# Kernel optimization log

Hardware: AMD Instinct MI355X
Metric: run time of the kernel (lower is better)

The kernel has to match this reference:

```python
import math
import jax, jax.numpy as jnp
import numpy as np

NUM_HEADS = 16
HEAD_DIM = 128
BLOCK = 256
EPS = 1e-6


def _get_slopes(n):
    def p2(n):
        start = 2 ** (-2 ** (-(math.log2(n) - 3)))
        return [start * start ** i for i in range(n)]
    if math.log2(n).is_integer():
        return p2(n)
    c = 2 ** math.floor(math.log2(n))
    return p2(c) + _get_slopes(2 * c)[0::2][: n - c]


def setup_inputs() -> dict:
    key = jax.random.key(0)
    ks = jax.random.split(key, 4)
    d_in, d_out = 2048, 2048
    x = jax.random.normal(ks[0], (2, 4096, d_in), dtype=jnp.float32)
    Wqkv = jax.random.normal(ks[1], (d_in, 3 * NUM_HEADS * HEAD_DIM), dtype=jnp.float32) * 0.02
    Wg = jax.random.normal(ks[2], (d_in, NUM_HEADS * HEAD_DIM), dtype=jnp.float32) * 0.02
    Wout = jax.random.normal(ks[3], (NUM_HEADS * HEAD_DIM, d_out), dtype=jnp.float32) * 0.02
    norm_w = jnp.ones((NUM_HEADS * HEAD_DIM,), dtype=jnp.float32)
    return {"x": x, "Wqkv": Wqkv, "Wg": Wg, "Wout": Wout, "norm_w": norm_w}


def reference(x, Wqkv, Wg, Wout, norm_w):
    b, n, _ = x.shape
    h, d = NUM_HEADS, HEAD_DIM
    nb = n // BLOCK  # seq_len chosen divisible by block_size

    # slopes (ALiBi-style), shape [h,1,1]
    slope = jnp.asarray(_get_slopes(h), dtype=jnp.float32).reshape(h, 1, 1)

    qkv = jax.nn.silu(x @ Wqkv)                       # [b,n,3hd]
    qkv = qkv.reshape(b, n, h, 3 * d)
    q, k, v = jnp.split(qkv, 3, axis=-1)              # each [b,n,h,d]
    q = q.transpose(0, 2, 1, 3)                       # [b,h,n,d]
    k = k.transpose(0, 2, 1, 3)
    v = v.transpose(0, 2, 1, 3)

    # per-position decay factors within a block
    arr = jnp.arange(BLOCK, dtype=jnp.float32) + 1.0          # [B]
    q_decay = jnp.exp(-slope * arr[:, None])                  # [h,B,1]
    k_decay = jnp.exp(-slope * (BLOCK - arr[:, None]))        # [h,B,1]
    idx = arr[:, None] - arr[None, :]                         # [B,B]
    diag_decay = jnp.where(idx >= 0, jnp.exp(-slope[None] * idx[None, None]), 0.0)  # [1,h,B,B]
    block_decay = jnp.exp(-slope * BLOCK)                     # [h,1,1]

    # blocked xs: [nb, b, h, B, d]
    def to_blocks(t):
        return t.reshape(b, h, nb, BLOCK, d).transpose(2, 0, 1, 3, 4)

    qb, kb, vb = to_blocks(q), to_blocks(k), to_blocks(v)

    def step(kv, blk):
        qi, ki, vi = blk                                       # [b,h,B,d]
        # inter-block: (qi * q_decay) @ kv  -> [b,h,B,d]
        non_diag = jnp.einsum('bhmd,bhde->bhme', qi * q_decay, kv)
        # intra-block causal decayed attention
        qk = jnp.einsum('bhmd,bhnd->bhmn', qi, ki) * diag_decay
        diag = jnp.einsum('bhmn,bhne->bhme', qk, vi)
        out = non_diag + diag
        kv_new = block_decay * kv + jnp.einsum('bhmd,bhme->bhde', ki * k_decay, vi)
        return kv_new, out

    kv0 = jnp.zeros((b, h, d, d), dtype=jnp.float32)
    _, out_blocks = jax.lax.scan(step, kv0, (qb, kb, vb))      # [nb,b,h,B,d]
    o = out_blocks.transpose(1, 2, 0, 3, 4).reshape(b, h, n, d)
    o = o.transpose(0, 2, 1, 3).reshape(b, n, h * d)           # [b,n,hd]

    # T5 (RMS) LayerNorm
    var = jnp.mean(o * o, axis=-1, keepdims=True)
    o = o * jax.lax.rsqrt(var + EPS) * norm_w

    # output gate and projection
    o = jax.nn.sigmoid(x @ Wg) * o
    return o @ Wout
```

## Files before the change

### kernel.cpp

```cpp
#include <hip/hip_runtime.h>
#include <cstddef>

typedef float f32x4 __attribute__((ext_vector_type(4)));
typedef __bf16 bf16x8 __attribute__((ext_vector_type(8)));
typedef unsigned short u16x8 __attribute__((ext_vector_type(8)));
typedef unsigned short u16x4 __attribute__((ext_vector_type(4)));

constexpr int NB = 2, S = 4096, H = 16, D = 128;
constexpr int DIN = 2048, NQKV = 6144, HD = 2048;
constexpr int BLK = 256, NBL = 16;

constexpr size_t SZ_XB    = (size_t)NB * S * DIN * 2;
constexpr size_t SZ_WQKVT = (size_t)NQKV * DIN * 2;
constexpr size_t SZ_WGT   = (size_t)HD * DIN * 2;
constexpr size_t SZ_WOUTT = (size_t)HD * HD * 2;
constexpr size_t SZ_QKVB  = (size_t)NB * S * NQKV * 2;
constexpr size_t SZ_GB    = (size_t)NB * S * HD * 2;
constexpr size_t SZ_ST    = (size_t)NB * H * NBL * D * D * 2;
constexpr size_t SZ_OB    = (size_t)NB * S * HD * 2;

__device__ __forceinline__ float bf2f(unsigned short u) {
  return __uint_as_float(((unsigned)u) << 16);
}
__device__ __forceinline__ unsigned short f2bf(float f) {
  unsigned u = __float_as_uint(f);
  u += 0x7fffu + ((u >> 16) & 1u);
  return (unsigned short)(u >> 16);
}
__device__ __forceinline__ void gload16(const void* g, void* l) {
  __builtin_amdgcn_global_load_lds(
      (const __attribute__((address_space(1))) unsigned int*)g,
      (__attribute__((address_space(3))) unsigned int*)l, 16, 0, 0);
}

__global__ __launch_bounds__(256) void cvt_bf16(
    const float* __restrict__ in, unsigned short* __restrict__ out) {
  const size_t id = (size_t)blockIdx.x * 256 + threadIdx.x;
  const float4 a = *(const float4*)&in[id * 8];
  const float4 c = *(const float4*)&in[id * 8 + 4];
  u16x8 o;
  o[0] = f2bf(a.x); o[1] = f2bf(a.y); o[2] = f2bf(a.z); o[3] = f2bf(a.w);
  o[4] = f2bf(c.x); o[5] = f2bf(c.y); o[6] = f2bf(c.z); o[7] = f2bf(c.w);
  *(u16x8*)&out[id * 8] = o;
}

__global__ __launch_bounds__(256) void transpose_cvt(
    const float* __restrict__ W, unsigned short* __restrict__ Wt, int K, int N) {
  __shared__ unsigned short tile[32][33];
  const int n0 = blockIdx.x * 32, k0 = blockIdx.y * 32;
  const int t = threadIdx.x;
  const int r = t >> 3, c4 = (t & 7) * 4;
  const float4 v = *(const float4*)&W[(size_t)(k0 + r) * N + n0 + c4];
  tile[r][c4 + 0] = f2bf(v.x);
  tile[r][c4 + 1] = f2bf(v.y);
  tile[r][c4 + 2] = f2bf(v.z);
  tile[r][c4 + 3] = f2bf(v.w);
  __syncthreads();
  u16x4 o;
  #pragma unroll
  for (int i = 0; i < 4; ++i) o[i] = tile[c4 + i][r];
  *(u16x4*)&Wt[(size_t)(n0 + r) * K + k0 + c4] = o;
}

template<int ACT>
__global__ __launch_bounds__(256, 4) void gemm128(
    const unsigned short* __restrict__ A, const unsigned short* __restrict__ Bt,
    void* __restrict__ O1, void* __restrict__ O2,
    int M, int N, int K, int NSPLIT) {
  __shared__ unsigned short lds[16384];
  char* ldsb = (char*)lds;
  const int t = threadIdx.x;
  const int lane = t & 63, wave = t >> 6;
  const int wr = wave >> 1, wc = wave & 1;
  const int l15 = lane & 15;

  const int nbm = M >> 7;
  const int nbmx = nbm >> 3;
  const int xcd = blockIdx.x & 7, q = blockIdx.x >> 3;
  const int bm = xcd * nbmx + (q % nbmx);
  const int bn = q / nbmx;

  const int cg = (t & 7) ^ ((t >> 3) & 7);
  const unsigned short* sA = A  + (size_t)(bm * 128 + (t >> 3)) * K + cg * 8;
  const unsigned short* sB = Bt + (size_t)(bn * 128 + (t >> 3)) * K + cg * 8;
  const int dstb = t << 4;

  int offA[2][4], offB[2][4];
  #pragma unroll
  for (int kk = 0; kk < 2; ++kk) {
    #pragma unroll
    for (int m = 0; m < 4; ++m) {
      const int row = wr * 64 + m * 16 + l15;
      offA[kk][m] = row * 128 + (((kk * 4 + (lane >> 4)) ^ (row & 7)) << 4);
    }
    #pragma unroll
    for (int n = 0; n < 4; ++n) {
      const int row = wc * 64 + n * 16 + l15;
      offB[kk][n] = 16384 + row * 128 + (((kk * 4 + (lane >> 4)) ^ (row & 7)) << 4);
    }
  }

  const int NT = K >> 6;
  f32x4 acc[4][4] = {};
  for (int u = 0; u < NT; ++u) {
    __syncthreads();
    const int ko = u * 64;
    #pragma unroll
    for (int i = 0; i < 4; ++i) {
      gload16(sA + (size_t)(i * 32) * K + ko, ldsb + i * 4096 + dstb);
      gload16(sB + (size_t)(i * 32) * K + ko, ldsb + 16384 + i * 4096 + dstb);
    }
    asm volatile("s_waitcnt vmcnt(0)" ::: "memory");
    __syncthreads();
    #pragma unroll
    for (int kk = 0; kk < 2; ++kk) {
      bf16x8 af[4], bfr[4];
      #pragma unroll
      for (int m = 0; m < 4; ++m) af[m] = *(const bf16x8*)(ldsb + offA[kk][m]);
      #pragma unroll
      for (int n = 0; n < 4; ++n) bfr[n] = *(const bf16x8*)(ldsb + offB[kk][n]);
      #pragma unroll
      for (int m = 0; m < 4; ++m)
        #pragma unroll
        for (int n = 0; n < 4; ++n)
          acc[m][n] = __builtin_amdgcn_mfma_f32_16x16x32_bf16(af[m], bfr[n], acc[m][n], 0, 0, 0);
    }
  }

  const int ro = (lane >> 4) * 4, co = l15;
  const bool lo = (bn * 128) < NSPLIT;
  #pragma unroll
  for (int m = 0; m < 4; ++m)
    #pragma unroll
    for (int n = 0; n < 4; ++n) {
      const int gc = bn * 128 + wc * 64 + n * 16 + co;
      #pragma unroll
      for (int r = 0; r < 4; ++r) {
        const int gr = bm * 128 + wr * 64 + m * 16 + ro + r;
        float v = acc[m][n][r];
        if constexpr (ACT == 0) {
          ((float*)O1)[(size_t)gr * N + gc] = v;
        } else {
          if (lo) {
            v = v / (1.f + __expf(-v));
            ((unsigned short*)O1)[(size_t)gr * NSPLIT + gc] = f2bf(v);
          } else {
            v = 1.f / (1.f + __expf(-v));
            ((unsigned short*)O2)[(size_t)gr * (N - NSPLIT) + (gc - NSPLIT)] = f2bf(v);
          }
        }
      }
    }
}

__global__ __launch_bounds__(256) void kv_outer(
    const unsigned short* __restrict__ qkv, unsigned short* __restrict__ st) {
  const int gid = blockIdx.x;
  const int j = gid & 15;
  const int bh = gid >> 4;
  const int h = bh & 15;
  const int b = bh >> 4;
  const float slope = exp2f(-0.5f * (float)(h + 1));
  const int t = threadIdx.x;
  const int lane = t & 63, wave = t >> 6, wr = wave >> 1, wc = wave & 1;
  const int l15 = lane & 15;
  __shared__ unsigned short vt[128][72];
  __shared__ unsigned short kt[128][72];
  f32x4 acc[4][4] = {};
  const int mm = t & 63;
  const int c0 = (t >> 6) * 32;
  for (int ch = 0; ch < 4; ++ch) {
    if (ch) __syncthreads();
    const int m = ch * 64 + mm;
    const int seq = b * S + j * BLK + m;
    const float kd = expf(-slope * (float)(255 - m));
    const unsigned short* row = &qkv[(size_t)seq * NQKV + h * 384];
    #pragma unroll
    for (int i = 0; i < 4; ++i) {
      const u16x8 k8 = *(const u16x8*)&row[128 + c0 + i * 8];
      const u16x8 v8 = *(const u16x8*)&row[256 + c0 + i * 8];
      #pragma unroll
      for (int q2 = 0; q2 < 8; ++q2) {
        kt[c0 + i * 8 + q2][mm] = f2bf(bf2f(k8[q2]) * kd);
        vt[c0 + i * 8 + q2][mm] = v8[q2];
      }
    }
    __syncthreads();
    #pragma unroll
    for (int kk = 0; kk < 2; ++kk) {
      bf16x8 af[4], bfr[4];
      #pragma unroll
      for (int mi = 0; mi < 4; ++mi)
        af[mi] = *(const bf16x8*)&vt[wr * 64 + mi * 16 + l15][kk * 32 + (lane >> 4) * 8];
      #pragma unroll
      for (int n = 0; n < 4; ++n)
        bfr[n] = *(const bf16x8*)&kt[wc * 64 + n * 16 + l15][kk * 32 + (lane >> 4) * 8];
      #pragma unroll
      for (int mi = 0; mi < 4; ++mi)
        #pragma unroll
        for (int n = 0; n < 4; ++n)
          acc[mi][n] = __builtin_amdgcn_mfma_f32_16x16x32_bf16(af[mi], bfr[n], acc[mi][n], 0, 0, 0);
    }
  }
  const size_t base = (size_t)gid * (D * D);
  const int ro = (lane >> 4) * 4;
  #pragma unroll
  for (int mi = 0; mi < 4; ++mi)
    #pragma unroll
    for (int n = 0; n < 4; ++n) {
      const int e = wc * 64 + n * 16 + l15;
      #pragma unroll
      for (int r = 0; r < 4; ++r) {
        const int f = wr * 64 + mi * 16 + ro + r;
        st[base + (size_t)f * D + e] = f2bf(acc[mi][n][r]);
      }
    }
}

__global__ __launch_bounds__(256) void kv_scan(unsigned short* __restrict__ st) {
  const int id = blockIdx.x * 256 + threadIdx.x;
  const int ef = id & (D * D - 1);
  const int bh = id >> 14;
  const int h = bh & 15;
  const float slope = exp2f(-0.5f * (float)(h + 1));
  const float bd = expf(-slope * 256.f);
  unsigned short* p = st + (size_t)bh * NBL * D * D + ef;
  float cur = 0.f;
  #pragma unroll
  for (int jj = 0; jj < NBL; ++jj) {
    const float m = bf2f(p[(size_t)jj * D * D]);
    p[(size_t)jj * D * D] = f2bf(cur);
    cur = bd * cur + m;
  }
}

__global__ __launch_bounds__(256, 2) void attn_mfma(
    const unsigned short* __restrict__ qkv, const unsigned short* __restrict__ st,
    unsigned short* __restrict__ ob) {
  const int gid = blockIdx.x;
  const int half = gid & 1;
  const int rest = gid >> 1;
  const int j = rest & 15;
  const int bh = rest >> 4;
  const int h = bh & 15;
  const int b = bh >> 4;
  const float slope = exp2f(-0.5f * (float)(h + 1));
  const int t = threadIdx.x;
  const int lane = t & 63, wave = t >> 6, wr = wave >> 1, wc = wave & 1;

  __shared__ unsigned short cb[128][136];
  __shared__ unsigned short pl[128][136];

  bf16x8 af[4][4];
  #pragma unroll
  for (int m = 0; m < 4; ++m) {
    const int seq = b * S + j * BLK + half * 128 + wr * 64 + m * 16 + (lane & 15);
    const unsigned short* qrow = &qkv[(size_t)seq * NQKV + h * 384];
    #pragma unroll
    for (int kk = 0; kk < 4; ++kk)
      af[kk][m] = *(const bf16x8*)&qrow[kk * 32 + (lane >> 4) * 8];
  }
  {
    const int r = t >> 4, c0 = (t & 15) * 8;
    const size_t stbase = (size_t)rest * (D * D);
    #pragma unroll
    for (int p = 0; p < 8; ++p)
      *(u16x8*)&cb[r + p * 16][c0] = *(const u16x8*)&st[stbase + (size_t)(r + p * 16) * D + c0];
  }
  __syncthreads();

  f32x4 acc[4][4] = {};
  #pragma unroll
  for (int kk = 0; kk < 4; ++kk) {
    bf16x8 bfr[4];
    #pragma unroll
    for (int n = 0; n < 4; ++n)
      bfr[n] = *(const bf16x8*)&cb[wc * 64 + n * 16 + (lane & 15)][kk * 32 + (lane >> 4) * 8];
    #pragma unroll
    for (int m = 0; m < 4; ++m)
      #pragma unroll
      for (int n = 0; n < 4; ++n)
        acc[m][n] = __builtin_amdgcn_mfma_f32_16x16x32_bf16(af[kk][m], bfr[n], acc[m][n], 0, 0, 0);
  }
  const int ro = (lane >> 4) * 4;
  #pragma unroll
  for (int m = 0; m < 4; ++m)
    #pragma unroll
    for (int r = 0; r < 4; ++r) {
      const int gm = half * 128 + wr * 64 + m * 16 + ro + r;
      const float qd = expf(-slope * (float)(gm + 1));
      #pragma unroll
      for (int n = 0; n < 4; ++n) acc[m][n][r] *= qd;
    }

  const int nch = 1 + half;
  for (int c = 0; c < nch; ++c) {
    __syncthreads();
    {
      const int r = t >> 4, c0 = (t & 15) * 8;
      #pragma unroll
      for (int p = 0; p < 8; ++p) {
        const int seq = b * S + j * BLK + c * 128 + r + p * 16;
        *(u16x8*)&cb[r + p * 16][c0] = *(const u16x8*)&qkv[(size_t)seq * NQKV + h * 384 + 128 + c0];
      }
    }
    __syncthreads();
    f32x4 sacc[4][4] = {};
    #pragma unroll
    for (int kk = 0; kk < 4; ++kk) {
      bf16x8 bfr[4];
      #pragma unroll
      for (int n = 0; n < 4; ++n)
        bfr[n] = *(const bf16x8*)&cb[wc * 64 + n * 16 + (lane & 15)][kk * 32 + (lane >> 4) * 8];
      #pragma unroll
      for (int m = 0; m < 4; ++m)
        #pragma unroll
        for (int n = 0; n < 4; ++n)
          sacc[m][n] = __builtin_amdgcn_mfma_f32_16x16x32_bf16(af[kk][m], bfr[n], sacc[m][n], 0, 0, 0);
    }
    #pragma unroll
    for (int m = 0; m < 4; ++m)
      #pragma unroll
      for (int n = 0; n < 4; ++n) {
        const int lc = wc * 64 + n * 16 + (lane & 15);
        const int gp = c * 128 + lc;
        #pragma unroll
        for (int r = 0; r < 4; ++r) {
          const int lm = wr * 64 + m * 16 + ro + r;
          const int gm = half * 128 + lm;
          const float dd = (gm >= gp) ? expf(-slope * (float)(gm - gp)) : 0.f;
          pl[lm][lc] = f2bf(sacc[m][n][r] * dd);
        }
      }
    __syncthreads();
    {
      const int vr = t & 15, vc0 = (t >> 4) * 8;
      #pragma unroll
      for (int p = 0; p < 8; ++p) {
        const int row = vr + p * 16;
        const int seq = b * S + j * BLK + c * 128 + row;
        const u16x8 vv = *(const u16x8*)&qkv[(size_t)seq * NQKV + h * 384 + 256 + vc0];
        #pragma unroll
        for (int i = 0; i < 8; ++i) cb[vc0 + i][row] = vv[i];
      }
    }
    __syncthreads();
    #pragma unroll
    for (int kk = 0; kk < 4; ++kk) {
      bf16x8 pf[4], bfr[4];
      #pragma unroll
      for (int m = 0; m < 4; ++m)
        pf[m] = *(const bf16x8*)&pl[wr * 64 + m * 16 + (lane & 15)][kk * 32 + (lane >> 4) * 8];
      #pragma unroll
      for (int n = 0; n < 4; ++n)
        bfr[n] = *(const bf16x8*)&cb[wc * 64 + n * 16 + (lane & 15)][kk * 32 + (lane >> 4) * 8];
      #pragma unroll
      for (int m = 0; m < 4; ++m)
        #pragma unroll
        for (int n = 0; n < 4; ++n)
          acc[m][n] = __builtin_amdgcn_mfma_f32_16x16x32_bf16(pf[m], bfr[n], acc[m][n], 0, 0, 0);
    }
  }

  #pragma unroll
  for (int m = 0; m < 4; ++m)
    #pragma unroll
    for (int n = 0; n < 4; ++n) {
      const int fc = h * D + wc * 64 + n * 16 + (lane & 15);
      #pragma unroll
      for (int r = 0; r < 4; ++r) {
        const int seq = b * S + j * BLK + half * 128 + wr * 64 + m * 16 + ro + r;
        ob[(size_t)seq * HD + fc] = f2bf(acc[m][n][r]);
      }
    }
}

__global__ __launch_bounds__(256) void norm_gate(
    const unsigned short* __restrict__ ob, const unsigned short* __restrict__ gb,
    const float* __restrict__ nw, unsigned short* __restrict__ og) {
  const int row = blockIdx.x;
  const int t = threadIdx.x;
  const u16x8 ov = *(const u16x8*)&ob[(size_t)row * HD + t * 8];
  float f[8];
  float ss = 0.f;
  #pragma unroll
  for (int i = 0; i < 8; ++i) { f[i] = bf2f(ov[i]); ss += f[i] * f[i]; }
  #pragma unroll
  for (int off = 32; off > 0; off >>= 1) ss += __shfl_down(ss, off, 64);
  __shared__ float red[4];
  if ((t & 63) == 0) red[t >> 6] = ss;
  __syncthreads();
  const float rms = rsqrtf((red[0] + red[1] + red[2] + red[3]) * (1.f / HD) + 1e-6f);
  const u16x8 gv = *(const u16x8*)&gb[(size_t)row * HD + t * 8];
  u16x8 ow;
  #pragma unroll
  for (int i = 0; i < 8; ++i)
    ow[i] = f2bf(f[i] * rms * nw[t * 8 + i] * bf2f(gv[i]));
  *(u16x8*)&og[(size_t)row * HD + t * 8] = ow;
}

extern "C" void kernel_launch(void* const* d_in, const int* in_sizes, int n_in,
                              void* d_out, int out_size, void* d_ws, size_t ws_size,
                              hipStream_t stream) {
  (void)in_sizes; (void)n_in; (void)out_size; (void)ws_size;
  const float* x    = (const float*)d_in[0];
  const float* Wqkv = (const float*)d_in[1];
  const float* Wg   = (const float*)d_in[2];
  const float* Wout = (const float*)d_in[3];
  const float* nw   = (const float*)d_in[4];

  char* ws = (char*)d_ws;
  unsigned short* xb    = (unsigned short*)ws; ws += SZ_XB;
  unsigned short* wqkvt = (unsigned short*)ws; ws += SZ_WQKVT;
  unsigned short* wgt   = (unsigned short*)ws; ws += SZ_WGT;
  unsigned short* woutt = (unsigned short*)ws; ws += SZ_WOUTT;
  unsigned short* qkvb  = (unsigned short*)ws; ws += SZ_QKVB;
  unsigned short* gb    = (unsigned short*)ws; ws += SZ_GB;
  unsigned short* st    = (unsigned short*)ws; ws += SZ_ST;
  unsigned short* ob    = (unsigned short*)ws; ws += SZ_OB;
  unsigned short* og    = xb;
  (void)wgt;

  cvt_bf16<<<dim3((NB * S * DIN) / (256 * 8)), 256, 0, stream>>>(x, xb);
  transpose_cvt<<<dim3(NQKV / 32, DIN / 32), 256, 0, stream>>>(Wqkv, wqkvt, DIN, NQKV);
  transpose_cvt<<<dim3(HD / 32, DIN / 32), 256, 0, stream>>>(Wg, wgt, DIN, HD);
  transpose_cvt<<<dim3(HD / 32, HD / 32), 256, 0, stream>>>(Wout, woutt, HD, HD);

  gemm128<3><<<dim3((NB * S / 128) * ((NQKV + HD) / 128)), 256, 0, stream>>>(
      xb, wqkvt, qkvb, gb, NB * S, NQKV + HD, DIN, NQKV);

  kv_outer<<<dim3(NB * H * NBL), 256, 0, stream>>>(qkvb, st);
  kv_scan<<<dim3((NB * H * D * D) / 256), 256, 0, stream>>>(st);
  attn_mfma<<<dim3(NB * H * NBL * 2), 256, 0, stream>>>(qkvb, st, ob);

  norm_gate<<<dim3(NB * S), 256, 0, stream>>>(ob, gb, nw, og);
  gemm128<0><<<dim3((NB * S / 128) * (HD / 128)), 256, 0, stream>>>(
      og, woutt, d_out, nullptr, NB * S, HD, HD, 0);
}
```

Before: 478.9 us.

## Load state and K fragments directly from global, prefetch V into registers

The attention kernel now reads the inter-block state and K operand fragments for MFMA straight from global memory instead of staging them through shared memory. V tiles are prefetched into registers before the QK^T MFMAs and written transposed to LDS afterwards. This removes several __syncthreads barriers per chunk and overlaps the V load latency with compute. The cost is uncoalesced, partly redundant global reads for the B fragments (each wave re-reads rows) and higher register pressure from vreg.

```diff
diff --git a/kernel.cpp b/kernel.cpp
--- a/kernel.cpp
+++ b/kernel.cpp
@@ -247,6 +247,7 @@
   const float slope = exp2f(-0.5f * (float)(h + 1));
   const int t = threadIdx.x;
   const int lane = t & 63, wave = t >> 6, wr = wave >> 1, wc = wave & 1;
+  const int l15 = lane & 15;
 
   __shared__ unsigned short cb[128][136];
   __shared__ unsigned short pl[128][136];
@@ -254,28 +255,21 @@
   bf16x8 af[4][4];
   #pragma unroll
   for (int m = 0; m < 4; ++m) {
-    const int seq = b * S + j * BLK + half * 128 + wr * 64 + m * 16 + (lane & 15);
+    const int seq = b * S + j * BLK + half * 128 + wr * 64 + m * 16 + l15;
     const unsigned short* qrow = &qkv[(size_t)seq * NQKV + h * 384];
     #pragma unroll
     for (int kk = 0; kk < 4; ++kk)
       af[kk][m] = *(const bf16x8*)&qrow[kk * 32 + (lane >> 4) * 8];
   }
-  {
-    const int r = t >> 4, c0 = (t & 15) * 8;
-    const size_t stbase = (size_t)rest * (D * D);
-    #pragma unroll
-    for (int p = 0; p < 8; ++p)
-      *(u16x8*)&cb[r + p * 16][c0] = *(const u16x8*)&st[stbase + (size_t)(r + p * 16) * D + c0];
-  }
-  __syncthreads();
 
   f32x4 acc[4][4] = {};
+  const unsigned short* stb = st + (size_t)rest * (D * D);
   #pragma unroll
   for (int kk = 0; kk < 4; ++kk) {
     bf16x8 bfr[4];
     #pragma unroll
     for (int n = 0; n < 4; ++n)
-      bfr[n] = *(const bf16x8*)&cb[wc * 64 + n * 16 + (lane & 15)][kk * 32 + (lane >> 4) * 8];
+      bfr[n] = *(const bf16x8*)&stb[(size_t)(wc * 64 + n * 16 + l15) * D + kk * 32 + (lane >> 4) * 8];
     #pragma unroll
     for (int m = 0; m < 4; ++m)
       #pragma unroll
@@ -294,24 +288,23 @@
     }
 
   const int nch = 1 + half;
+  const int vr = t & 15, vc0 = (t >> 4) * 8;
   for (int c = 0; c < nch; ++c) {
-    __syncthreads();
-    {
-      const int r = t >> 4, c0 = (t & 15) * 8;
-      #pragma unroll
-      for (int p = 0; p < 8; ++p) {
-        const int seq = b * S + j * BLK + c * 128 + r + p * 16;
-        *(u16x8*)&cb[r + p * 16][c0] = *(const u16x8*)&qkv[(size_t)seq * NQKV + h * 384 + 128 + c0];
-      }
-    }
-    __syncthreads();
+    u16x8 vreg[8];
+    #pragma unroll
+    for (int p = 0; p < 8; ++p) {
+      const int seq = b * S + j * BLK + c * 128 + vr + p * 16;
+      vreg[p] = *(const u16x8*)&qkv[(size_t)seq * NQKV + h * 384 + 256 + vc0];
+    }
     f32x4 sacc[4][4] = {};
     #pragma unroll
     for (int kk = 0; kk < 4; ++kk) {
       bf16x8 bfr[4];
       #pragma unroll
-      for (int n = 0; n < 4; ++n)
-        bfr[n] = *(const bf16x8*)&cb[wc * 64 + n * 16 + (lane & 15)][kk * 32 + (lane >> 4) * 8];
+      for (int n = 0; n < 4; ++n) {
+        const int seq = b * S + j * BLK + c * 128 + wc * 64 + n * 16 + l15;
+        bfr[n] = *(const bf16x8*)&qkv[(size_t)seq * NQKV + h * 384 + 128 + kk * 32 + (lane >> 4) * 8];
+      }
       #pragma unroll
       for (int m = 0; m < 4; ++m)
         #pragma unroll
@@ -319,10 +312,14 @@
           sacc[m][n] = __builtin_amdgcn_mfma_f32_16x16x32_bf16(af[kk][m], bfr[n], sacc[m][n], 0, 0, 0);
     }
     #pragma unroll
+    for (int p = 0; p < 8; ++p)
+      #pragma unroll
+      for (int i = 0; i < 8; ++i) cb[vc0 + i][vr + p * 16] = vreg[p][i];
+    #pragma unroll
     for (int m = 0; m < 4; ++m)
       #pragma unroll
       for (int n = 0; n < 4; ++n) {
-        const int lc = wc * 64 + n * 16 + (lane & 15);
+        const int lc = wc * 64 + n * 16 + l15;
         const int gp = c * 128 + lc;
         #pragma unroll
         for (int r = 0; r < 4; ++r) {
@@ -333,40 +330,29 @@
         }
       }
     __syncthreads();
-    {
-      const int vr = t & 15, vc0 = (t >> 4) * 8;
-      #pragma unroll
-      for (int p = 0; p < 8; ++p) {
-        const int row = vr + p * 16;
-        const int seq = b * S + j * BLK + c * 128 + row;
-        const u16x8 vv = *(const u16x8*)&qkv[(size_t)seq * NQKV + h * 384 + 256 + vc0];
-        #pragma unroll
-        for (int i = 0; i < 8; ++i) cb[vc0 + i][row] = vv[i];
-      }
-    }
-    __syncthreads();
     #pragma unroll
     for (int kk = 0; kk < 4; ++kk) {
       bf16x8 pf[4], bfr[4];
       #pragma unroll
       for (int m = 0; m < 4; ++m)
-        pf[m] = *(const bf16x8*)&pl[wr * 64 + m * 16 + (lane & 15)][kk * 32 + (lane >> 4) * 8];
+        pf[m] = *(const bf16x8*)&pl[wr * 64 + m * 16 + l15][kk * 32 + (lane >> 4) * 8];
       #pragma unroll
       for (int n = 0; n < 4; ++n)
-        bfr[n] = *(const bf16x8*)&cb[wc * 64 + n * 16 + (lane & 15)][kk * 32 + (lane >> 4) * 8];
+        bfr[n] = *(const bf16x8*)&cb[wc * 64 + n * 16 + l15][kk * 32 + (lane >> 4) * 8];
       #pragma unroll
       for (int m = 0; m < 4; ++m)
         #pragma unroll
         for (int n = 0; n < 4; ++n)
           acc[m][n] = __builtin_amdgcn_mfma_f32_16x16x32_bf16(pf[m], bfr[n], acc[m][n], 0, 0, 0);
     }
+    __syncthreads();
   }
 
   #pragma unroll
   for (int m = 0; m < 4; ++m)
     #pragma unroll
     for (int n = 0; n < 4; ++n) {
-      const int fc = h * D + wc * 64 + n * 16 + (lane & 15);
+      const int fc = h * D + wc * 64 + n * 16 + l15;
       #pragma unroll
       for (int r = 0; r < 4; ++r) {
         const int seq = b * S + j * BLK + half * 128 + wr * 64 + m * 16 + ro + r;
```

Result: slower. 489.8 us (+2.3%).
